# Performance work log

Hardware: AMD Instinct MI355X
Metric: run time of the kernel (lower is better)

Reference implementation:

```python
import jax, jax.numpy as jnp
import numpy as np

PS = 16          # patch_size
E = 256          # embed_dim
NH = 4           # num_heads
THR = 1.5        # entropy_threshold (bits)
LN_EPS = 1e-5


def _ln(x, g, b):
    m = x.mean(-1, keepdims=True)
    v = ((x - m) ** 2).mean(-1, keepdims=True)
    return (x - m) / jnp.sqrt(v + LN_EPS) * g + b


def _forward(video, conv_w, conv_b, wq_w, wq_b, wk_w, wk_b, wv_w, wv_b,
             lnq_g, lnq_b, lnk_g, lnk_b, lnv_g, lnv_b,
             in_proj_w, in_proj_b, out_proj_w, out_proj_b,
             dense_w, dense_b, bproj_w, bproj_b, group_query, ent_table):
    # Conv3d(3->E, k=(3,PS,PS), s=(2,PS,PS), p=(1,0,0)) + ReLU
    x = jax.lax.conv_general_dilated(
        video, conv_w, window_strides=(2, PS, PS),
        padding=((1, 1), (0, 0), (0, 0)),
        dimension_numbers=('NCDHW', 'OIDHW', 'NCDHW'))
    x = jax.nn.relu(x + conv_b[None, :, None, None, None])
    B = x.shape[0]
    tokens = x.reshape(B, E, -1).transpose(0, 2, 1)  # [B, N, E]
    N = tokens.shape[1]

    # per-token byte (no_grad in torch)
    byte = jax.lax.stop_gradient(
        jnp.clip(jnp.round(tokens.mean(-1) * 255.0), 0, 255)).astype(jnp.int32)  # [B, N]
    # entropy predictor: probs = softmax(ent_table[last_byte]) (last byte of running seq)
    logits = ent_table[byte[0]]                      # [N, 256]
    p = jax.nn.softmax(logits, axis=-1)
    ent = -(p * jnp.log2(p + 1e-9)).sum(-1)          # [N]
    boundary = (ent > THR).astype(jnp.int32)
    seg = jnp.cumsum(boundary) - boundary            # exclusive cumsum -> segment id per token

    # DecoderCrossAttention with a single shared group_query per segment
    q0 = jnp.broadcast_to(group_query, (B, 1, E))    # byte_representations
    query = _ln(q0 @ wq_w.T + wq_b, lnq_g, lnq_b)    # [B,1,E]
    k = _ln(tokens @ wk_w.T + wk_b, lnk_g, lnk_b)    # [B,N,E]
    v = _ln(tokens @ wv_w.T + wv_b, lnv_g, lnv_b)

    Wqi, Wki, Wvi = in_proj_w[:E], in_proj_w[E:2 * E], in_proj_w[2 * E:]
    bqi, bki, bvi = in_proj_b[:E], in_proj_b[E:2 * E], in_proj_b[2 * E:]
    dh = E // NH
    qp = ((query @ Wqi.T + bqi) * (dh ** -0.5)).reshape(B, NH, dh)  # [B,H,dh]
    kp = (k @ Wki.T + bki).reshape(B, N, NH, dh)
    vp = (v @ Wvi.T + bvi).reshape(B, N, NH, dh)

    scores = jnp.einsum('bhd,bnhd->nbh', qp, kp)     # [N,B,H]
    smax = jax.ops.segment_max(scores, seg, num_segments=N)   # [N,B,H]
    w = jnp.exp(scores - smax[seg])
    denom = jax.ops.segment_sum(w, seg, num_segments=N)       # [N,B,H]
    num = jax.ops.segment_sum(w[..., None] * vp.transpose(1, 0, 2, 3),
                              seg, num_segments=N)            # [N,B,H,dh]
    count = jax.ops.segment_sum(jnp.ones((N,), scores.dtype), seg, num_segments=N)
    valid = count > 0
    safe = jnp.where(valid[:, None, None], denom, 1.0)
    attn = (num / safe[..., None]).transpose(1, 0, 2, 3).reshape(B, N, E)
    out = attn @ out_proj_w.T + out_proj_b
    out = out @ dense_w.T + dense_b
    out = out + q0                                   # residual with byte_representations
    patches = out @ bproj_w.T + bproj_b              # binary_proj
    return jnp.where(valid[None, :, None], patches, 0.0)  # [B, N, E] padded


def setup_inputs() -> dict:
    key = jax.random.key(0)
    ks = jax.random.split(key, 16)
    rn = lambda k, s, sc=0.02: jax.random.normal(k, s, jnp.float32) * sc
    z = lambda *s: jnp.zeros(s, jnp.float32)
    o = lambda *s: jnp.ones(s, jnp.float32)
    return {
        'video': jax.random.normal(ks[0], (4, 3, 32, 224, 224), jnp.float32),
        'conv_w': rn(ks[1], (E, 3, 3, PS, PS)), 'conv_b': z(E),
        'wq_w': rn(ks[2], (E, E)), 'wq_b': z(E),
        'wk_w': rn(ks[3], (E, E)), 'wk_b': z(E),
        'wv_w': rn(ks[4], (E, E)), 'wv_b': z(E),
        'lnq_g': o(E), 'lnq_b': z(E),
        'lnk_g': o(E), 'lnk_b': z(E),
        'lnv_g': o(E), 'lnv_b': z(E),
        'in_proj_w': rn(ks[5], (3 * E, E)), 'in_proj_b': z(3 * E),
        'out_proj_w': rn(ks[6], (E, E)), 'out_proj_b': z(E),
        'dense_w': rn(ks[7], (E, E)), 'dense_b': z(E),
        'bproj_w': rn(ks[8], (E, E)), 'bproj_b': z(E),
        'group_query': jax.random.normal(ks[9], (1, 1, E), jnp.float32),
        'ent_table': jax.random.normal(ks[10], (256, 256), jnp.float32) * 6.0,
    }


def reference(video, conv_w, conv_b, wq_w, wq_b, wk_w, wk_b, wv_w, wv_b,
              lnq_g, lnq_b, lnk_g, lnk_b, lnv_g, lnv_b,
              in_proj_w, in_proj_b, out_proj_w, out_proj_b,
              dense_w, dense_b, bproj_w, bproj_b, group_query, ent_table):
    return _forward(video, conv_w, conv_b, wq_w, wq_b, wk_w, wk_b, wv_w, wv_b,
                    lnq_g, lnq_b, lnk_g, lnk_b, lnv_g, lnv_b,
                    in_proj_w, in_proj_b, out_proj_w, out_proj_b,
                    dense_w, dense_b, bproj_w, bproj_b, group_query, ent_table)
```

## Files before the change

kernel.cpp:

```cpp
#include <hip/hip_runtime.h>
#include <hip/hip_bf16.h>
#include <math.h>

#define NTOK 3136
#define MT 12544
#define KCV 2304
#define THRESH 1.5f
#define LN_EPS 1e-5f

typedef short short8 __attribute__((ext_vector_type(8)));
typedef float f32x4 __attribute__((ext_vector_type(4)));

__device__ __forceinline__ unsigned short f2bf(float f) {
    unsigned int u = __float_as_uint(f);
    u += 0x7fffu + ((u >> 16) & 1u);
    return (unsigned short)(u >> 16);
}
__device__ __forceinline__ float bf2f(unsigned short h) {
    return __uint_as_float(((unsigned int)h) << 16);
}
__device__ __forceinline__ unsigned int cvt_pk_bf16(float x0, float x1) {
    union { __hip_bfloat162 h; unsigned int u; } cv;
    cv.h = __float22bfloat162_rn(make_float2(x0, x1));
    return cv.u;
}
__device__ __forceinline__ void async16(const void* g, void* l) {
    __builtin_amdgcn_global_load_lds((const __attribute__((address_space(1))) void*)g,
                                     (__attribute__((address_space(3))) void*)l, 16, 0, 0);
}

__device__ __forceinline__ float wsum(float v) {
#pragma unroll
    for (int o = 32; o > 0; o >>= 1) v += __shfl_xor(v, o);
    return v;
}
__device__ __forceinline__ float wmax(float v) {
#pragma unroll
    for (int o = 32; o > 0; o >>= 1) v = fmaxf(v, __shfl_xor(v, o));
    return v;
}

__global__ __launch_bounds__(256) void split_cw_k(const float* __restrict__ cw,
    unsigned short* __restrict__ cwh, unsigned short* __restrict__ cwl)
{
    int i = blockIdx.x * 256 + threadIdx.x;
    int e = i & 255, kg = i >> 8;
    if (kg >= 288) return;
    const float4* sp = (const float4*)(cw + (size_t)e * KCV + kg * 8);
    float4 x0 = sp[0], x1 = sp[1];
    float av[8] = {x0.x, x0.y, x0.z, x0.w, x1.x, x1.y, x1.z, x1.w};
    short8 hh, ll;
#pragma unroll
    for (int j = 0; j < 8; ++j) {
        unsigned short h = f2bf(av[j]);
        hh[j] = (short)h;
        ll[j] = (short)f2bf(av[j] - bf2f(h));
    }
    size_t off = (size_t)kg * 2048 + e * 8;
    *(short8*)&cwh[off] = hh;
    *(short8*)&cwl[off] = ll;
}

__global__ __launch_bounds__(256) void cast_w_k(
    const float* __restrict__ s0, const float* __restrict__ s1, const float* __restrict__ s2,
    const float* __restrict__ s3, const float* __restrict__ s4, const float* __restrict__ s5,
    unsigned short* __restrict__ dst)
{
    int i = blockIdx.x * 256 + threadIdx.x;
    if (i >= 524288) return;
    float v;
    if      (i <  65536) v = s0[i];
    else if (i < 131072) v = s1[i - 65536];
    else if (i < 327680) v = s2[i - 131072];
    else if (i < 393216) v = s3[i - 327680];
    else if (i < 458752) v = s4[i - 393216];
    else                 v = s5[i - 458752];
    dst[i] = f2bf(v);
}

__global__ __launch_bounds__(256) void conv_mfma_k(
    const float* __restrict__ video, const unsigned short* __restrict__ cwh,
    const unsigned short* __restrict__ cwl, const float* __restrict__ cbias,
    float* __restrict__ tokmean4, unsigned short* __restrict__ outB)
{
    __shared__ __align__(16) unsigned short Bh[8192], Bl[8192];
    const int t    = threadIdx.x;
    const int lane = t & 63;
    const int w    = t >> 6;
    const int l15  = lane & 15, lq = lane >> 4;
    const int v_  = blockIdx.x;
    const int s_  = (v_ & 7) * 98 + (v_ >> 3);
    const int mb  = s_ >> 2, eb = s_ & 3;
    const int m0  = mb * 64, e0 = eb * 64;

    const int m = m0 + w * 16 + l15;
    const int b = m / NTOK, n = m % NTOK;
    const int d = n / 196, hw = n % 196;
    const int h = hw / 14, ww = hw % 14;
    const float* vb = video + (size_t)(b * 3) * (32 * 50176) + (h * 16) * 224 + ww * 16;
    const int dbase = 2 * d - 1;

    f32x4 acc[4] = {};
    float4 a0, a1, a2, a3, b0, b1, b2, b3;

#define STAGE_B(s, buf)                                                              \
    {                                                                                \
        _Pragma("unroll")                                                            \
        for (int r_ = 0; r_ < 2; ++r_) {                                             \
            const int kgl = w + r_ * 4;                                              \
            const size_t gsrc = (size_t)((s) * 8 + kgl) * 2048 + (e0 + lane) * 8;    \
            async16(cwh + gsrc, &Bh[(buf) * 4096 + kgl * 512]);                      \
            async16(cwl + gsrc, &Bl[(buf) * 4096 + kgl * 512]);                      \
        }                                                                            \
    }
#define LOAD_A32(k0v, x0, x1)                                                        \
    {                                                                                \
        const int k0  = (k0v) + lq * 8;                                              \
        const int c   = k0 / 768;                                                    \
        const int rem = k0 - c * 768;                                                \
        const int kd  = rem >> 8;                                                    \
        const int r2  = rem & 255;                                                   \
        const int id  = dbase + kd;                                                  \
        x0 = make_float4(0.f, 0.f, 0.f, 0.f); x1 = x0;                               \
        if (id >= 0) {                                                               \
            const float* p = vb + (size_t)c * (32 * 50176) + id * 50176 +            \
                             (r2 >> 4) * 224 + (r2 & 15);                            \
            x0 = *(const float4*)p;                                                  \
            x1 = *(const float4*)(p + 4);                                            \
        }                                                                            \
    }
#define CVT_AB(y0, y1, fah, fal)                                                     \
    short8 fah, fal;                                                                 \
    {                                                                                \
        float av[8] = {y0.x, y0.y, y0.z, y0.w, y1.x, y1.y, y1.z, y1.w};              \
        unsigned int ph[4], pl[4];                                                   \
        _Pragma("unroll")                                                            \
        for (int j = 0; j < 4; ++j) {                                                \
            float u0 = av[2 * j], u1 = av[2 * j + 1];                                \
            unsigned int hu = cvt_pk_bf16(u0, u1);                                   \
            float r0 = u0 - __uint_as_float(hu << 16);                               \
            float r1 = u1 - __uint_as_float(hu & 0xffff0000u);                       \
            ph[j] = hu;                                                              \
            pl[j] = cvt_pk_bf16(r0, r1);                                             \
        }                                                                            \
        int4 phv = make_int4(ph[0], ph[1], ph[2], ph[3]);                            \
        int4 plv = make_int4(pl[0], pl[1], pl[2], pl[3]);                            \
        fah = *(short8*)&phv;                                                        \
        fal = *(short8*)&plv;                                                        \
    }

    STAGE_B(0, 0);
    LOAD_A32(0, a0, a1);
    LOAD_A32(32, a2, a3);
    __syncthreads();

    for (int s = 0; s < 36; ++s) {
        const int cbuf = s & 1;
        if (s + 1 < 36) {
            STAGE_B(s + 1, cbuf ^ 1);
            LOAD_A32((s + 1) * 64,      b0, b1);
            LOAD_A32((s + 1) * 64 + 32, b2, b3);
        }
        {
            CVT_AB(a0, a1, fah, fal);
            const int rb = cbuf * 4096 + lq * 512 + l15 * 8;
#pragma unroll
            for (int ct = 0; ct < 4; ++ct) {
                short8 fbh = *(const short8*)&Bh[rb + ct * 128];
                short8 fbl = *(const short8*)&Bl[rb + ct * 128];
                acc[ct] = __builtin_amdgcn_mfma_f32_16x16x32_bf16(fah, fbh, acc[ct], 0, 0, 0);
                acc[ct] = __builtin_amdgcn_mfma_f32_16x16x32_bf16(fah, fbl, acc[ct], 0, 0, 0);
                acc[ct] = __builtin_amdgcn_mfma_f32_16x16x32_bf16(fal, fbh, acc[ct], 0, 0, 0);
            }
        }
        {
            CVT_AB(a2, a3, fah, fal);
            const int rb = cbuf * 4096 + (4 + lq) * 512 + l15 * 8;
#pragma unroll
            for (int ct = 0; ct < 4; ++ct) {
                short8 fbh = *(const short8*)&Bh[rb + ct * 128];
                short8 fbl = *(const short8*)&Bl[rb + ct * 128];
                acc[ct] = __builtin_amdgcn_mfma_f32_16x16x32_bf16(fah, fbh, acc[ct], 0, 0, 0);
                acc[ct] = __builtin_amdgcn_mfma_f32_16x16x32_bf16(fah, fbl, acc[ct], 0, 0, 0);
                acc[ct] = __builtin_amdgcn_mfma_f32_16x16x32_bf16(fal, fbh, acc[ct], 0, 0, 0);
            }
        }
        __syncthreads();
        a0 = b0; a1 = b1; a2 = b2; a3 = b3;
    }
#undef STAGE_B
#undef LOAD_A32
#undef CVT_AB

    const int rbase = m0 + w * 16 + lq * 4;
    float rsum[4] = {0.f, 0.f, 0.f, 0.f};
#pragma unroll
    for (int ct = 0; ct < 4; ++ct) {
        int e = e0 + ct * 16 + l15;
        float bias = cbias[e];
#pragma unroll
        for (int r = 0; r < 4; ++r) {
            float vv = fmaxf(acc[ct][r] + bias, 0.f);
            outB[(size_t)(rbase + r) * 256 + e] = f2bf(vv);
            rsum[r] += vv;
        }
    }
    if (m0 < NTOK) {
#pragma unroll
        for (int r = 0; r < 4; ++r) {
            float sv = rsum[r];
            sv += __shfl_xor(sv, 1); sv += __shfl_xor(sv, 2);
            sv += __shfl_xor(sv, 4); sv += __shfl_xor(sv, 8);
            if (l15 == 0) tokmean4[(size_t)eb * NTOK + rbase + r] = sv;
        }
    }
}

__global__ __launch_bounds__(256) void gemm_single_k(
    const unsigned short* __restrict__ A, const unsigned short* __restrict__ W,
    const float* __restrict__ bias, const float* __restrict__ addvec,
    const int* __restrict__ Sptr, float* __restrict__ outF, unsigned short* __restrict__ outB)
{
    __shared__ __align__(16) unsigned short As[8192], Bs[8192];
    const int t = threadIdx.x, lane = t & 63, w = t >> 6;
    const int v_ = blockIdx.x;
    const int s_ = (v_ & 7) * 98 + (v_ >> 3);
    const int m0 = (s_ >> 2) * 64, e0 = (s_ & 3) * 64;
    const int l15 = lane & 15, lq = lane >> 4;
    const unsigned short* ga = A + (size_t)(m0 + lane) * 256;
    const unsigned short* gb = W + (size_t)(e0 + lane) * 256;
#pragma unroll
    for (int kg = w; kg < 16; kg += 4) {
        async16(ga + kg * 8, &As[kg * 512]);
        async16(gb + kg * 8, &Bs[kg * 512]);
    }
    f32x4 acc[4] = {};
    __syncthreads();
    ;
    int S = Sptr ? *Sptr : 0x7fffffff;
#pragma unroll
    for (int s = 0; s < 4; ++s) {
        int kg = s * 4 + lq;
        short8 a = *(const short8*)&As[(kg & 15) * 512 + (w * 16 + l15) * 8];
        short8 a_dummy = a; (void)a_dummy;
        break;
    }
#pragma unroll
    for (int s = 0; s < 4; ++s) {
        int kg = s * 4 + lq;
        short8 a = *(const short8*)&As[kg * 512 + (w * 16 + l15) * 8];
#pragma unroll
        for (int ct = 0; ct < 4; ++ct) {
            short8 bb = *(const short8*)&Bs[kg * 512 + (ct * 16 + l15) * 8];
            acc[ct] = __builtin_amdgcn_mfma_f32_16x16x32_bf16(a, bb, acc[ct], 0, 0, 0);
        }
    }
    __syncthreads();
#pragma unroll
    for (int kg = w; kg < 16; kg += 4) {
        async16(ga + (16 + kg) * 8, &As[kg * 512]);
        async16(gb + (16 + kg) * 8, &Bs[kg * 512]);
    }
    __syncthreads();
#pragma unroll
    for (int s = 0; s < 4; ++s) {
        int kg = s * 4 + lq;
        short8 a = *(const short8*)&As[kg * 512 + (w * 16 + l15) * 8];
#pragma unroll
        for (int ct = 0; ct < 4; ++ct) {
            short8 bb = *(const short8*)&Bs[kg * 512 + (ct * 16 + l15) * 8];
            acc[ct] = __builtin_amdgcn_mfma_f32_16x16x32_bf16(a, bb, acc[ct], 0, 0, 0);
        }
    }
    int rbase = m0 + w * 16 + lq * 4;
#pragma unroll
    for (int ct = 0; ct < 4; ++ct) {
        int e = e0 + ct * 16 + l15;
        float bv = bias[e] + (addvec ? addvec[e] : 0.f);
#pragma unroll
        for (int r = 0; r < 4; ++r) {
            int mm = rbase + r;
            float vv = acc[ct][r] + bv;
            if ((mm % NTOK) >= S) vv = 0.f;
            size_t off = (size_t)mm * 256 + e;
            if (outF) outF[off] = vv;
            if (outB) outB[off] = f2bf(vv);
        }
    }
}

__global__ __launch_bounds__(256) void gemm_dual_k(
    const unsigned short* __restrict__ A0, const unsigned short* __restrict__ A1,
    const unsigned short* __restrict__ W,
    const float* __restrict__ bias0, const float* __restrict__ bias1,
    unsigned short* __restrict__ outB0, unsigned short* __restrict__ outB1)
{
    __shared__ __align__(16) unsigned short As[8192], Bs[8192];
    const int t = threadIdx.x, lane = t & 63, w = t >> 6;
    const int v_ = blockIdx.x;
    const int s_ = (v_ & 7) * 196 + (v_ >> 3);
    const int mb = s_ >> 3, ebg = s_ & 7;
    const int half = ebg >> 2;
    const unsigned short* A = half ? A1 : A0;
    const float* bias = half ? bias1 : bias0;
    unsigned short* outB = half ? outB1 : outB0;
    const int m0 = mb * 64, eg0 = ebg * 64, el0 = (ebg & 3) * 64;
    const int l15 = lane & 15, lq = lane >> 4;
    const unsigned short* ga = A + (size_t)(m0 + lane) * 256;
    const unsigned short* gb = W + (size_t)(eg0 + lane) * 256;
#pragma unroll
    for (int kg = w; kg < 16; kg += 4) {
        async16(ga + kg * 8, &As[kg * 512]);
        async16(gb + kg * 8, &Bs[kg * 512]);
    }
    f32x4 acc[4] = {};
    __syncthreads();
#pragma unroll
    for (int s = 0; s < 4; ++s) {
        int kg = s * 4 + lq;
        short8 a = *(const short8*)&As[kg * 512 + (w * 16 + l15) * 8];
#pragma unroll
        for (int ct = 0; ct < 4; ++ct) {
            short8 bb = *(const short8*)&Bs[kg * 512 + (ct * 16 + l15) * 8];
            acc[ct] = __builtin_amdgcn_mfma_f32_16x16x32_bf16(a, bb, acc[ct], 0, 0, 0);
        }
    }
    __syncthreads();
#pragma unroll
    for (int kg = w; kg < 16; kg += 4) {
        async16(ga + (16 + kg) * 8, &As[kg * 512]);
        async16(gb + (16 + kg) * 8, &Bs[kg * 512]);
    }
    __syncthreads();
#pragma unroll
    for (int s = 0; s < 4; ++s) {
        int kg = s * 4 + lq;
        short8 a = *(const short8*)&As[kg * 512 + (w * 16 + l15) * 8];
#pragma unroll
        for (int ct = 0; ct < 4; ++ct) {
            short8 bb = *(const short8*)&Bs[kg * 512 + (ct * 16 + l15) * 8];
            acc[ct] = __builtin_amdgcn_mfma_f32_16x16x32_bf16(a, bb, acc[ct], 0, 0, 0);
        }
    }
    int rbase = m0 + w * 16 + lq * 4;
#pragma unroll
    for (int ct = 0; ct < 4; ++ct) {
        int e = el0 + ct * 16 + l15;
        float bv = bias[e];
#pragma unroll
        for (int r = 0; r < 4; ++r) {
            float vv = acc[ct][r] + bv;
            outB[(size_t)(rbase + r) * 256 + e] = f2bf(vv);
        }
    }
}

__global__ __launch_bounds__(256) void boundary_k(
    const float* __restrict__ tokmean4, const float* __restrict__ ent_table,
    int* __restrict__ boundary)
{
    int n    = blockIdx.x * 4 + (threadIdx.x >> 6);
    int lane = threadIdx.x & 63;
    float s0 = tokmean4[n];
    float s1 = tokmean4[NTOK + n];
    float s2 = tokmean4[2 * NTOK + n];
    float s3 = tokmean4[3 * NTOK + n];
    float mean = ((s0 + s1) + (s2 + s3)) * (1.f / 256.f);
    float bf = rintf(mean * 255.f);
    bf = fminf(fmaxf(bf, 0.f), 255.f);
    int byte = (int)bf;
    const float4 lg = reinterpret_cast<const float4*>(ent_table + byte * 256)[lane];
    float mx = wmax(fmaxf(fmaxf(lg.x, lg.y), fmaxf(lg.z, lg.w)));
    float e0 = expf(lg.x - mx), e1 = expf(lg.y - mx), e2 = expf(lg.z - mx), e3 = expf(lg.w - mx);
    float z = wsum(e0 + e1 + e2 + e3);
    float iz = 1.f / z;
    float p0 = e0 * iz, p1 = e1 * iz, p2 = e2 * iz, p3 = e3 * iz;
    float ep = -(p0 * log2f(p0 + 1e-9f) + p1 * log2f(p1 + 1e-9f) +
                 p2 * log2f(p2 + 1e-9f) + p3 * log2f(p3 + 1e-9f));
    ep = wsum(ep);
    if (lane == 0) boundary[n] = (ep > THRESH) ? 1 : 0;
}

__global__ __launch_bounds__(256) void scan_k(const int* __restrict__ boundary,
    int* __restrict__ seg_start, int* __restrict__ Sptr)
{
    __shared__ int sums[256];
    const int t = threadIdx.x;
    const int CH = 13;
    int base = t * CH;
    int s = 0;
    for (int i = 0; i < CH; i++) { int n = base + i; if (n < NTOK) s += boundary[n]; }
    sums[t] = s; __syncthreads();
    for (int o = 1; o < 256; o <<= 1) {
        int v = sums[t];
        int u = (t >= o) ? sums[t - o] : 0;
        __syncthreads();
        sums[t] = v + u;
        __syncthreads();
    }
    int run = (t == 0) ? 0 : sums[t - 1];
    if (t == 0) seg_start[0] = 0;
    for (int i = 0; i < CH; i++) {
        int n = base + i;
        if (n >= NTOK) break;
        int v = boundary[n];
        if (n == NTOK - 1) { Sptr[0] = run + 1; seg_start[run + 1] = NTOK; }
        if (v && (n + 1 < NTOK)) seg_start[run + 1] = n + 1;
        run += v;
    }
}

__global__ __launch_bounds__(256) void lnKV_k(
    const unsigned short* __restrict__ Pk, const unsigned short* __restrict__ Pv,
    const float* __restrict__ gk, const float* __restrict__ bk,
    const float* __restrict__ gv, const float* __restrict__ bv,
    unsigned short* __restrict__ Yk, unsigned short* __restrict__ Yv)
{
    int row  = blockIdx.x * 4 + (threadIdx.x >> 6);
    int lane = threadIdx.x & 63;
    int half = row >= MT;
    int r    = half ? row - MT : row;
    const unsigned short* X = half ? Pv : Pk;
    const float* g = half ? gv : gk;
    const float* b = half ? bv : bk;
    unsigned short* Y = half ? Yv : Yk;
    ushort4 xr = reinterpret_cast<const ushort4*>(X + (size_t)r * 256)[lane];
    float x0 = bf2f(xr.x), x1 = bf2f(xr.y), x2 = bf2f(xr.z), x3 = bf2f(xr.w);
    float m = wsum(x0 + x1 + x2 + x3) * (1.f / 256.f);
    float d0 = x0 - m, d1 = x1 - m, d2 = x2 - m, d3 = x3 - m;
    float var = wsum(d0 * d0 + d1 * d1 + d2 * d2 + d3 * d3) * (1.f / 256.f);
    float inv = 1.f / sqrtf(var + LN_EPS);
    float4 g4 = reinterpret_cast<const float4*>(g)[lane];
    float4 b4 = reinterpret_cast<const float4*>(b)[lane];
    ushort4 y;
    y.x = f2bf(d0 * inv * g4.x + b4.x);
    y.y = f2bf(d1 * inv * g4.y + b4.y);
    y.z = f2bf(d2 * inv * g4.z + b4.z);
    y.w = f2bf(d3 * inv * g4.w + b4.w);
    reinterpret_cast<ushort4*>(Y + (size_t)r * 256)[lane] = y;
}

__global__ __launch_bounds__(256) void query_k(
    const float* __restrict__ gq, const float* __restrict__ wq_w, const float* __restrict__ wq_b,
    const float* __restrict__ lnq_g, const float* __restrict__ lnq_b,
    const float* __restrict__ inW, const float* __restrict__ inB, float* __restrict__ qp)
{
    __shared__ float sh[256];
    __shared__ float red[256];
    const int t = threadIdx.x;
    float acc = wq_b[t];
    for (int j = 0; j < 256; j++) acc += gq[j] * wq_w[t * 256 + j];
    red[t] = acc; __syncthreads();
    for (int o = 128; o > 0; o >>= 1) { if (t < o) red[t] += red[t + o]; __syncthreads(); }
    float m = red[0] * (1.f / 256.f);
    __syncthreads();
    float d = acc - m;
    red[t] = d * d; __syncthreads();
    for (int o = 128; o > 0; o >>= 1) { if (t < o) red[t] += red[t + o]; __syncthreads(); }
    float inv = 1.f / sqrtf(red[0] * (1.f / 256.f) + LN_EPS);
    sh[t] = d * inv * lnq_g[t] + lnq_b[t];
    __syncthreads();
    float a2 = inB[t];
    for (int j = 0; j < 256; j++) a2 += sh[j] * inW[t * 256 + j];
    qp[t] = a2 * 0.125f;
}

__global__ __launch_bounds__(256) void scores_k(const unsigned short* __restrict__ kp,
    const float* __restrict__ qp, float* __restrict__ sc)
{
    int idx  = blockIdx.x * 4 + (threadIdx.x >> 6);
    int lane = threadIdx.x & 63;
    ushort4 k4 = reinterpret_cast<const ushort4*>(kp + (size_t)idx * 256)[lane];
    float4 q4 = reinterpret_cast<const float4*>(qp)[lane];
    float p = bf2f(k4.x) * q4.x + bf2f(k4.y) * q4.y + bf2f(k4.z) * q4.z + bf2f(k4.w) * q4.w;
    p += __shfl_xor(p, 1); p += __shfl_xor(p, 2);
    p += __shfl_xor(p, 4); p += __shfl_xor(p, 8);
    if ((lane & 15) == 0) {
        int b = idx / NTOK, n = idx % NTOK;
        int h = lane >> 4;
        sc[(b * 4 + h) * NTOK + n] = p;
    }
}

__global__ __launch_bounds__(256) void attn_bf_k(const float* __restrict__ sc,
    const unsigned short* __restrict__ vp, const int* __restrict__ seg_start,
    const int* __restrict__ Sptr, unsigned short* __restrict__ attn)
{
    int s    = blockIdx.x;
    int b    = threadIdx.x >> 6;
    int lane = threadIdx.x & 63;
    unsigned short* orow = attn + ((size_t)b * NTOK + s) * 256;
    int S = *Sptr;
    if (s >= S) {
#pragma unroll
        for (int h = 0; h < 4; h++) orow[h * 64 + lane] = 0;
        return;
    }
    int st = seg_start[s], en = seg_start[s + 1];
    for (int h = 0; h < 4; h++) {
        const float* scr = sc + (b * 4 + h) * NTOK;
        float m = -1e30f;
        for (int n = st; n < en; n++) m = fmaxf(m, scr[n]);
        float den = 0.f, acc = 0.f;
        for (int n = st; n < en; n++) {
            float wgt = expf(scr[n] - m);
            den += wgt;
            acc += wgt * bf2f(vp[((size_t)b * NTOK + n) * 256 + h * 64 + lane]);
        }
        orow[h * 64 + lane] = f2bf(acc / den);
    }
}

extern "C" void kernel_launch(void* const* d_in, const int* in_sizes, int n_in,
                              void* d_out, int out_size, void* d_ws, size_t ws_size,
                              hipStream_t stream)
{
    const float* video      = (const float*)d_in[0];
    const float* conv_w     = (const float*)d_in[1];
    const float* conv_b     = (const float*)d_in[2];
    const float* wq_w       = (const float*)d_in[3];
    const float* wq_b       = (const float*)d_in[4];
    const float* wk_w       = (const float*)d_in[5];
    const float* wk_b       = (const float*)d_in[6];
    const float* wv_w       = (const float*)d_in[7];
    const float* wv_b       = (const float*)d_in[8];
    const float* lnq_g      = (const float*)d_in[9];
    const float* lnq_b      = (const float*)d_in[10];
    const float* lnk_g      = (const float*)d_in[11];
    const float* lnk_b      = (const float*)d_in[12];
    const float* lnv_g      = (const float*)d_in[13];
    const float* lnv_b      = (const float*)d_in[14];
    const float* in_proj_w  = (const float*)d_in[15];
    const float* in_proj_b  = (const float*)d_in[16];
    const float* out_proj_w = (const float*)d_in[17];
    const float* out_proj_b = (const float*)d_in[18];
    const float* dense_w    = (const float*)d_in[19];
    const float* dense_b    = (const float*)d_in[20];
    const float* bproj_w    = (const float*)d_in[21];
    const float* bproj_b    = (const float*)d_in[22];
    const float* group_q    = (const float*)d_in[23];
    const float* ent_table  = (const float*)d_in[24];
    float* out = (float*)d_out;

    float* tokmean4 = (float*)d_ws;
    unsigned short* Pk  = (unsigned short*)(tokmean4 + 16384);
    unsigned short* Pv  = Pk  + (size_t)MT * 256;
    unsigned short* B1  = Pv  + (size_t)MT * 256;
    unsigned short* B2k = B1  + (size_t)MT * 256;
    unsigned short* B2v = B2k + (size_t)MT * 256;
    unsigned short* B3k = B2v + (size_t)MT * 256;
    unsigned short* B3v = B3k + (size_t)MT * 256;
    unsigned short* cwh = B3v + (size_t)MT * 256;
    unsigned short* cwl = cwh + 256 * KCV;
    unsigned short* wpool = cwl + 256 * KCV;
    float* sc = (float*)(wpool + 524288);
    float* qp = sc + 16 * NTOK;
    int* boundary  = (int*)(qp + 256);
    int* seg_start = boundary + NTOK;
    int* Sp        = seg_start + (NTOK + 1);

    const unsigned short* inpb   = wpool + 131072;
    const unsigned short* outpb  = wpool + 327680;
    const unsigned short* denseb = wpool + 393216;
    const unsigned short* bprojb = wpool + 458752;

    dim3 blk(256);
    split_cw_k<<<dim3(288), blk, 0, stream>>>(conv_w, cwh, cwl);
    cast_w_k<<<dim3(2048), blk, 0, stream>>>(wk_w, wv_w, in_proj_w, out_proj_w,
                                             dense_w, bproj_w, wpool);
    conv_mfma_k<<<dim3(784), blk, 0, stream>>>(video, cwh, cwl, conv_b, tokmean4, B1);
    boundary_k<<<dim3(NTOK / 4), blk, 0, stream>>>(tokmean4, ent_table, boundary);
    scan_k<<<dim3(1), blk, 0, stream>>>(boundary, seg_start, Sp);
    query_k<<<dim3(1), blk, 0, stream>>>(group_q, wq_w, wq_b, lnq_g, lnq_b,
                                         in_proj_w, in_proj_b, qp);
    gemm_dual_k<<<dim3(1568), blk, 0, stream>>>(B1, B1, wpool, wk_b, wv_b, Pk, Pv);
    lnKV_k<<<dim3(2 * MT / 4), blk, 0, stream>>>(Pk, Pv, lnk_g, lnk_b, lnv_g, lnv_b,
                                                 B2k, B2v);
    gemm_dual_k<<<dim3(1568), blk, 0, stream>>>(B2k, B2v, inpb + 65536,
                                                in_proj_b + 256, in_proj_b + 512,
                                                B3k, B3v);
    scores_k<<<dim3(MT / 4), blk, 0, stream>>>(B3k, qp, sc);
    attn_bf_k<<<dim3(NTOK), blk, 0, stream>>>(sc, B3v, seg_start, Sp, B1);
    gemm_single_k<<<dim3(784), blk, 0, stream>>>(B1, outpb, out_proj_b,
                                                 nullptr, nullptr, nullptr, B2k);
    gemm_single_k<<<dim3(784), blk, 0, stream>>>(B2k, denseb, dense_b,
                                                 group_q, nullptr, nullptr, B2v);
    gemm_single_k<<<dim3(784), blk, 0, stream>>>(B2v, bprojb, bproj_b,
                                                 nullptr, Sp, out, nullptr);
}
```

Measured before the change: 354.2 us.

## Fuse prep kernels, fold scores into K projection GEMM, parallelize attention per head

Merges the conv-weight split, weight cast and query projection into a single prep kernel. The per-head score dot product is computed in the epilogue of the K in-projection GEMM, so the K projection output buffer and the separate scores kernel are no longer needed. The attention kernel launches one block per (segment, batch) with one wave per head instead of looping over heads. Conv B-tile staging changes from async global-to-LDS loads to register loads followed by LDS stores after the MFMA loop. Together these cut launch count and HBM traffic, at the cost of more register pressure in the conv kernel and a branchy GEMM epilogue.

```diff
diff --git a/kernel.cpp b/kernel.cpp
--- a/kernel.cpp
+++ b/kernel.cpp
@@ -40,42 +40,65 @@
     return v;
 }
 
-__global__ __launch_bounds__(256) void split_cw_k(const float* __restrict__ cw,
-    unsigned short* __restrict__ cwh, unsigned short* __restrict__ cwl)
-{
-    int i = blockIdx.x * 256 + threadIdx.x;
-    int e = i & 255, kg = i >> 8;
-    if (kg >= 288) return;
-    const float4* sp = (const float4*)(cw + (size_t)e * KCV + kg * 8);
-    float4 x0 = sp[0], x1 = sp[1];
-    float av[8] = {x0.x, x0.y, x0.z, x0.w, x1.x, x1.y, x1.z, x1.w};
-    short8 hh, ll;
-#pragma unroll
-    for (int j = 0; j < 8; ++j) {
-        unsigned short h = f2bf(av[j]);
-        hh[j] = (short)h;
-        ll[j] = (short)f2bf(av[j] - bf2f(h));
-    }
-    size_t off = (size_t)kg * 2048 + e * 8;
-    *(short8*)&cwh[off] = hh;
-    *(short8*)&cwl[off] = ll;
-}
-
-__global__ __launch_bounds__(256) void cast_w_k(
+__global__ __launch_bounds__(256) void prep_k(
+    const float* __restrict__ cw, unsigned short* __restrict__ cwh,
+    unsigned short* __restrict__ cwl,
     const float* __restrict__ s0, const float* __restrict__ s1, const float* __restrict__ s2,
     const float* __restrict__ s3, const float* __restrict__ s4, const float* __restrict__ s5,
-    unsigned short* __restrict__ dst)
-{
-    int i = blockIdx.x * 256 + threadIdx.x;
-    if (i >= 524288) return;
-    float v;
-    if      (i <  65536) v = s0[i];
-    else if (i < 131072) v = s1[i - 65536];
-    else if (i < 327680) v = s2[i - 131072];
-    else if (i < 393216) v = s3[i - 327680];
-    else if (i < 458752) v = s4[i - 393216];
-    else                 v = s5[i - 458752];
-    dst[i] = f2bf(v);
+    unsigned short* __restrict__ dst,
+    const float* __restrict__ gq, const float* __restrict__ wq_w,
+    const float* __restrict__ wq_b, const float* __restrict__ lnq_g,
+    const float* __restrict__ lnq_b, const float* __restrict__ inW,
+    const float* __restrict__ inB, float* __restrict__ qp)
+{
+    const int blk = blockIdx.x;
+    if (blk < 288) {
+        int i = blk * 256 + threadIdx.x;
+        int e = i & 255, kg = i >> 8;
+        const float4* sp = (const float4*)(cw + (size_t)e * KCV + kg * 8);
+        float4 x0 = sp[0], x1 = sp[1];
+        float av[8] = {x0.x, x0.y, x0.z, x0.w, x1.x, x1.y, x1.z, x1.w};
+        short8 hh, ll;
+#pragma unroll
+        for (int j = 0; j < 8; ++j) {
+            unsigned short h = f2bf(av[j]);
+            hh[j] = (short)h;
+            ll[j] = (short)f2bf(av[j] - bf2f(h));
+        }
+        size_t off = (size_t)kg * 2048 + e * 8;
+        *(short8*)&cwh[off] = hh;
+        *(short8*)&cwl[off] = ll;
+    } else if (blk < 2336) {
+        int i = (blk - 288) * 256 + threadIdx.x;
+        if (i >= 524288) return;
+        float v;
+        if      (i <  65536) v = s0[i];
+        else if (i < 131072) v = s1[i - 65536];
+        else if (i < 327680) v = s2[i - 131072];
+        else if (i < 393216) v = s3[i - 327680];
+        else if (i < 458752) v = s4[i - 393216];
+        else                 v = s5[i - 458752];
+        dst[i] = f2bf(v);
+    } else {
+        __shared__ float sh[256];
+        __shared__ float red[256];
+        const int t = threadIdx.x;
+        float acc = wq_b[t];
+        for (int j = 0; j < 256; j++) acc += gq[j] * wq_w[t * 256 + j];
+        red[t] = acc; __syncthreads();
+        for (int o = 128; o > 0; o >>= 1) { if (t < o) red[t] += red[t + o]; __syncthreads(); }
+        float m = red[0] * (1.f / 256.f);
+        __syncthreads();
+        float d = acc - m;
+        red[t] = d * d; __syncthreads();
+        for (int o = 128; o > 0; o >>= 1) { if (t < o) red[t] += red[t + o]; __syncthreads(); }
+        float inv = 1.f / sqrtf(red[0] * (1.f / 256.f) + LN_EPS);
+        sh[t] = d * inv * lnq_g[t] + lnq_b[t];
+        __syncthreads();
+        float a2 = inB[t];
+        for (int j = 0; j < 256; j++) a2 += sh[j] * inW[t * 256 + j];
+        qp[t] = a2 * 0.125f;
+    }
 }
 
 __global__ __launch_bounds__(256) void conv_mfma_k(
@@ -102,16 +125,24 @@
 
     f32x4 acc[4] = {};
     float4 a0, a1, a2, a3, b0, b1, b2, b3;
-
-#define STAGE_B(s, buf)                                                              \
+    short8 rh0, rh1, rl0, rl1;
+
+#define BLOAD(s)                                                                     \
     {                                                                                \
-        _Pragma("unroll")                                                            \
-        for (int r_ = 0; r_ < 2; ++r_) {                                             \
-            const int kgl = w + r_ * 4;                                              \
-            const size_t gsrc = (size_t)((s) * 8 + kgl) * 2048 + (e0 + lane) * 8;    \
-            async16(cwh + gsrc, &Bh[(buf) * 4096 + kgl * 512]);                      \
-            async16(cwl + gsrc, &Bl[(buf) * 4096 + kgl * 512]);                      \
-        }                                                                            \
+        const size_t g0 = (size_t)((s) * 8 + w) * 2048 + (e0 + lane) * 8;            \
+        const size_t g1 = g0 + 4 * 2048;                                             \
+        rh0 = *(const short8*)(cwh + g0);                                            \
+        rh1 = *(const short8*)(cwh + g1);                                            \
+        rl0 = *(const short8*)(cwl + g0);                                            \
+        rl1 = *(const short8*)(cwl + g1);                                            \
+    }
+#define BSTORE(buf)                                                                  \
+    {                                                                                \
+        const int o = (buf) * 4096 + w * 512 + lane * 8;                             \
+        *(short8*)&Bh[o]        = rh0;                                               \
+        *(short8*)&Bh[o + 2048] = rh1;                                               \
+        *(short8*)&Bl[o]        = rl0;                                               \
+        *(short8*)&Bl[o + 2048] = rl1;                                               \
     }
 #define LOAD_A32(k0v, x0, x1)                                                        \
     {                                                                                \
@@ -149,15 +180,16 @@
         fal = *(short8*)&plv;                                                        \
     }
 
-    STAGE_B(0, 0);
+    BLOAD(0);
     LOAD_A32(0, a0, a1);
     LOAD_A32(32, a2, a3);
+    BSTORE(0);
     __syncthreads();
 
     for (int s = 0; s < 36; ++s) {
         const int cbuf = s & 1;
         if (s + 1 < 36) {
-            STAGE_B(s + 1, cbuf ^ 1);
+            BLOAD(s + 1);
             LOAD_A32((s + 1) * 64,      b0, b1);
             LOAD_A32((s + 1) * 64 + 32, b2, b3);
         }
@@ -185,10 +217,12 @@
                 acc[ct] = __builtin_amdgcn_mfma_f32_16x16x32_bf16(fal, fbh, acc[ct], 0, 0, 0);
             }
         }
+        if (s + 1 < 36) BSTORE(cbuf ^ 1);
         __syncthreads();
         a0 = b0; a1 = b1; a2 = b2; a3 = b3;
     }
-#undef STAGE_B
+#undef BLOAD
+#undef BSTORE
 #undef LOAD_A32
 #undef CVT_AB
 
@@ -236,15 +270,6 @@
     }
     f32x4 acc[4] = {};
     __syncthreads();
-    ;
-    int S = Sptr ? *Sptr : 0x7fffffff;
-#pragma unroll
-    for (int s = 0; s < 4; ++s) {
-        int kg = s * 4 + lq;
-        short8 a = *(const short8*)&As[(kg & 15) * 512 + (w * 16 + l15) * 8];
-        short8 a_dummy = a; (void)a_dummy;
-        break;
-    }
 #pragma unroll
     for (int s = 0; s < 4; ++s) {
         int kg = s * 4 + lq;
@@ -272,6 +297,7 @@
             acc[ct] = __builtin_amdgcn_mfma_f32_16x16x32_bf16(a, bb, acc[ct], 0, 0, 0);
         }
     }
+    int S = Sptr ? *Sptr : 0x7fffffff;
     int rbase = m0 + w * 16 + lq * 4;
 #pragma unroll
     for (int ct = 0; ct < 4; ++ct) {
@@ -293,7 +319,8 @@
     const unsigned short* __restrict__ A0, const unsigned short* __restrict__ A1,
     const unsigned short* __restrict__ W,
     const float* __restrict__ bias0, const float* __restrict__ bias1,
-    unsigned short* __restrict__ outB0, unsigned short* __restrict__ outB1)
+    unsigned short* __restrict__ outB0, unsigned short* __restrict__ outB1,
+    const float* __restrict__ qp, float* __restrict__ sc)
 {
     __shared__ __align__(16) unsigned short As[8192], Bs[8192];
     const int t = threadIdx.x, lane = t & 63, w = t >> 6;
@@ -343,14 +370,39 @@
         }
     }
     int rbase = m0 + w * 16 + lq * 4;
-#pragma unroll
-    for (int ct = 0; ct < 4; ++ct) {
-        int e = el0 + ct * 16 + l15;
-        float bv = bias[e];
+    if (qp && half == 0) {
+        float sp[4] = {0.f, 0.f, 0.f, 0.f};
+#pragma unroll
+        for (int ct = 0; ct < 4; ++ct) {
+            int e = el0 + ct * 16 + l15;
+            float bv = bias[e];
+            float qv = qp[e];
+#pragma unroll
+            for (int r = 0; r < 4; ++r) sp[r] += (acc[ct][r] + bv) * qv;
+        }
 #pragma unroll
         for (int r = 0; r < 4; ++r) {
-            float vv = acc[ct][r] + bv;
-            outB[(size_t)(rbase + r) * 256 + e] = f2bf(vv);
+            sp[r] += __shfl_xor(sp[r], 1); sp[r] += __shfl_xor(sp[r], 2);
+            sp[r] += __shfl_xor(sp[r], 4); sp[r] += __shfl_xor(sp[r], 8);
+        }
+        if (l15 == 0) {
+#pragma unroll
+            for (int r = 0; r < 4; ++r) {
+                int mm = rbase + r;
+                int bb = mm / NTOK, nn = mm % NTOK;
+                sc[(bb * 4 + ebg) * NTOK + nn] = sp[r];
+            }
+        }
+    } else {
+#pragma unroll
+        for (int ct = 0; ct < 4; ++ct) {
+            int e = el0 + ct * 16 + l15;
+            float bv = bias[e];
+#pragma unroll
+            for (int r = 0; r < 4; ++r) {
+                float vv = acc[ct][r] + bv;
+                outB[(size_t)(rbase + r) * 256 + e] = f2bf(vv);
+            }
         }
     }
 }
@@ -440,75 +492,29 @@
     reinterpret_cast<ushort4*>(Y + (size_t)r * 256)[lane] = y;
 }
 
-__global__ __launch_bounds__(256) void query_k(
-    const float* __restrict__ gq, const float* __restrict__ wq_w, const float* __restrict__ wq_b,
-    const float* __restrict__ lnq_g, const float* __restrict__ lnq_b,
-    const float* __restrict__ inW, const float* __restrict__ inB, float* __restrict__ qp)
-{
-    __shared__ float sh[256];
-    __shared__ float red[256];
-    const int t = threadIdx.x;
-    float acc = wq_b[t];
-    for (int j = 0; j < 256; j++) acc += gq[j] * wq_w[t * 256 + j];
-    red[t] = acc; __syncthreads();
-    for (int o = 128; o > 0; o >>= 1) { if (t < o) red[t] += red[t + o]; __syncthreads(); }
-    float m = red[0] * (1.f / 256.f);
-    __syncthreads();
-    float d = acc - m;
-    red[t] = d * d; __syncthreads();
-    for (int o = 128; o > 0; o >>= 1) { if (t < o) red[t] += red[t + o]; __syncthreads(); }
-    float inv = 1.f / sqrtf(red[0] * (1.f / 256.f) + LN_EPS);
-    sh[t] = d * inv * lnq_g[t] + lnq_b[t];
-    __syncthreads();
-    float a2 = inB[t];
-    for (int j = 0; j < 256; j++) a2 += sh[j] * inW[t * 256 + j];
-    qp[t] = a2 * 0.125f;
-}
-
-__global__ __launch_bounds__(256) void scores_k(const unsigned short* __restrict__ kp,
-    const float* __restrict__ qp, float* __restrict__ sc)
-{
-    int idx  = blockIdx.x * 4 + (threadIdx.x >> 6);
-    int lane = threadIdx.x & 63;
-    ushort4 k4 = reinterpret_cast<const ushort4*>(kp + (size_t)idx * 256)[lane];
-    float4 q4 = reinterpret_cast<const float4*>(qp)[lane];
-    float p = bf2f(k4.x) * q4.x + bf2f(k4.y) * q4.y + bf2f(k4.z) * q4.z + bf2f(k4.w) * q4.w;
-    p += __shfl_xor(p, 1); p += __shfl_xor(p, 2);
-    p += __shfl_xor(p, 4); p += __shfl_xor(p, 8);
-    if ((lane & 15) == 0) {
-        int b = idx / NTOK, n = idx % NTOK;
-        int h = lane >> 4;
-        sc[(b * 4 + h) * NTOK + n] = p;
-    }
-}
-
 __global__ __launch_bounds__(256) void attn_bf_k(const float* __restrict__ sc,
     const unsigned short* __restrict__ vp, const int* __restrict__ seg_start,
     const int* __restrict__ Sptr, unsigned short* __restrict__ attn)
 {
     int s    = blockIdx.x;
-    int b    = threadIdx.x >> 6;
+    int b    = blockIdx.y;
+    int h    = threadIdx.x >> 6;
     int lane = threadIdx.x & 63;
     unsigned short* orow = attn + ((size_t)b * NTOK + s) * 256;
     int S = *Sptr;
-    if (s >= S) {
-#pragma unroll
-        for (int h = 0; h < 4; h++) orow[h * 64 + lane] = 0;
-        return;
-    }
+    if (s >= S) { orow[h * 64 + lane] = 0; return; }
     int st = seg_start[s], en = seg_start[s + 1];
-    for (int h = 0; h < 4; h++) {
-        const float* scr = sc + (b * 4 + h) * NTOK;
-        float m = -1e30f;
-        for (int n = st; n < en; n++) m = fmaxf(m, scr[n]);
-        float den = 0.f, acc = 0.f;
-        for (int n = st; n < en; n++) {
-            float wgt = expf(scr[n] - m);
-            den += wgt;
-            acc += wgt * bf2f(vp[((size_t)b * NTOK + n) * 256 + h * 64 + lane]);
-        }
-        orow[h * 64 + lane] = f2bf(acc / den);
-    }
+    const float* scr = sc + (b * 4 + h) * NTOK;
+    float m = -1e30f;
+    for (int n = st; n < en; n++) m = fmaxf(m, scr[n]);
+    float den = 0.f, acc = 0.f;
+    const unsigned short* vpb = vp + (size_t)b * NTOK * 256 + h * 64 + lane;
+    for (int n = st; n < en; n++) {
+        float wgt = expf(scr[n] - m);
+        den += wgt;
+        acc += wgt * bf2f(vpb[(size_t)n * 256]);
+    }
+    orow[h * 64 + lane] = f2bf(acc / den);
 }
 
 extern "C" void kernel_launch(void* const* d_in, const int* in_sizes, int n_in,
@@ -548,8 +554,7 @@
     unsigned short* B1  = Pv  + (size_t)MT * 256;
     unsigned short* B2k = B1  + (size_t)MT * 256;
     unsigned short* B2v = B2k + (size_t)MT * 256;
-    unsigned short* B3k = B2v + (size_t)MT * 256;
-    unsigned short* B3v = B3k + (size_t)MT * 256;
+    unsigned short* B3v = B2v + (size_t)MT * 256;
     unsigned short* cwh = B3v + (size_t)MT * 256;
     unsigned short* cwl = cwh + 256 * KCV;
     unsigned short* wpool = cwl + 256 * KCV;
@@ -565,22 +570,22 @@
     const unsigned short* bprojb = wpool + 458752;
 
     dim3 blk(256);
-    split_cw_k<<<dim3(288), blk, 0, stream>>>(conv_w, cwh, cwl);
-    cast_w_k<<<dim3(2048), blk, 0, stream>>>(wk_w, wv_w, in_proj_w, out_proj_w,
-                                             dense_w, bproj_w, wpool);
+    prep_k<<<dim3(2337), blk, 0, stream>>>(conv_w, cwh, cwl,
+                                           wk_w, wv_w, in_proj_w, out_proj_w,
+                                           dense_w, bproj_w, wpool,
+                                           group_q, wq_w, wq_b, lnq_g, lnq_b,
+                                           in_proj_w, in_proj_b, qp);
     conv_mfma_k<<<dim3(784), blk, 0, stream>>>(video, cwh, cwl, conv_b, tokmean4, B1);
     boundary_k<<<dim3(NTOK / 4), blk, 0, stream>>>(tokmean4, ent_table, boundary);
     scan_k<<<dim3(1), blk, 0, stream>>>(boundary, seg_start, Sp);
-    query_k<<<dim3(1), blk, 0, stream>>>(group_q, wq_w, wq_b, lnq_g, lnq_b,
-                                         in_proj_w, in_proj_b, qp);
-    gemm_dual_k<<<dim3(1568), blk, 0, stream>>>(B1, B1, wpool, wk_b, wv_b, Pk, Pv);
+    gemm_dual_k<<<dim3(1568), blk, 0, stream>>>(B1, B1, wpool, wk_b, wv_b, Pk, Pv,
+                                                nullptr, nullptr);
     lnKV_k<<<dim3(2 * MT / 4), blk, 0, stream>>>(Pk, Pv, lnk_g, lnk_b, lnv_g, lnv_b,
                                                  B2k, B2v);
     gemm_dual_k<<<dim3(1568), blk, 0, stream>>>(B2k, B2v, inpb + 65536,
                                                 in_proj_b + 256, in_proj_b + 512,
-                                                B3k, B3v);
-    scores_k<<<dim3(MT / 4), blk, 0, stream>>>(B3k, qp, sc);
-    attn_bf_k<<<dim3(NTOK), blk, 0, stream>>>(sc, B3v, seg_start, Sp, B1);
+                                                nullptr, B3v, qp, sc);
+    attn_bf_k<<<dim3(NTOK, 4), blk, 0, stream>>>(sc, B3v, seg_start, Sp, B1);
     gemm_single_k<<<dim3(784), blk, 0, stream>>>(B1, outpb, out_proj_b,
                                                  nullptr, nullptr, nullptr, B2k);
     gemm_single_k<<<dim3(784), blk, 0, stream>>>(B2k, denseb, dense_b,
```

Result: faster. 329.3 us (-7.0%).
